# Performance work log

Measured on AMD Instinct MI355X. Metric: run time of the kernel, lower is better.

Reference implementation:

```python
import jax, jax.numpy as jnp
import numpy as np

DIM = 256
HEADS = 8
DIM_HEAD = 64
INNER = HEADS * DIM_HEAD  # 512
K = 7   # kv conv kernel == stride
P = 7   # local patch size
B = 2
N = 3584  # divisible by P and K; l = L = 512


def setup_inputs() -> dict:
    key = jax.random.key(0)
    ks = jax.random.split(key, 5)
    x = jax.random.normal(ks[0], (B, DIM, N), jnp.float32)
    # Conv1d weights (bias=False for q/kv, bias for out), kaiming-ish scale
    w_q = jax.random.normal(ks[1], (INNER, DIM), jnp.float32) * (1.0 / np.sqrt(DIM))
    w_kv = jax.random.normal(ks[2], (2 * INNER, DIM, K), jnp.float32) * (1.0 / np.sqrt(DIM * K))
    w_out = jax.random.normal(ks[3], (DIM, INNER), jnp.float32) * (1.0 / np.sqrt(INNER))
    b_out = jax.random.normal(ks[4], (DIM,), jnp.float32) * 0.01
    return {"x": x, "w_q": w_q, "w_kv": w_kv, "w_out": w_out, "b_out": b_out}


def reference(x, w_q, w_kv, w_out, b_out):
    b, c, n = x.shape
    h, d, p, kk = HEADS, DIM_HEAD, P, K
    l = n // p            # number of local query patches
    L = n // kk           # downsampled global K/V length
    scale = d ** -0.5

    # to_q: 1x1 conv (pointwise) -- same whether applied per-patch or on full seq
    q = jnp.einsum('oc,bcn->bon', w_q, x)                      # (b, inner, n)
    q = q.reshape(b, h, d, l, p).transpose(0, 3, 1, 4, 2)      # (b, l, h, p, d)

    # to_kv: Conv1d kernel=k, stride=k -> non-overlapping block contraction
    xk = x.reshape(b, c, L, kk)                                # (b, c, L, k)
    kv = jnp.einsum('ocj,bclj->bol', w_kv, xk)                 # (b, 2*inner, L)
    k_, v_ = jnp.split(kv, 2, axis=1)
    k_ = k_.reshape(b, h, d, L).transpose(0, 1, 3, 2)          # (b, h, L, d)
    v_ = v_.reshape(b, h, d, L).transpose(0, 1, 3, 2)          # (b, h, L, d)

    # Faithful to torch: q batch order is (b, l, h) while k.repeat(l,1,1)
    # gives order (l, b, h). With b | l, query (bb, ll, hh) attends to
    # K/V of batch (ll mod b), head hh. Express via reshape of l -> (l//b, b)
    # so the repeated K/V is never materialized.
    assert l % b == 0, "faithful repeat-pairing requires b | l"
    q_r = q.reshape(b, l // b, b, h, p, d)                     # e-axis = ll mod b
    dots = jnp.einsum('acehpd,ehjd->acehpj', q_r, k_) * scale  # (b, l//b, b, h, p, L)
    attn = jax.nn.softmax(dots, axis=-1)
    out = jnp.einsum('acehpj,ehjd->acehpd', attn, v_)          # (b, l//b, b, h, p, d)

    # '(b l h) p d -> b (h d) (l p)'
    out = out.reshape(b, l, h, p, d).transpose(0, 2, 4, 1, 3).reshape(b, h * d, n)

    # to_out: 1x1 conv with bias (dropout=0 -> identity)
    return jnp.einsum('oc,bcn->bon', w_out, out) + b_out[None, :, None]
```

## Files before the change

kernel.cpp:

```cpp
#include <hip/hip_runtime.h>
#include <cmath>

#define DIM 256
#define N_SEQ 3584
#define INNER 512
#define HEADS 8
#define DHEAD 64
#define LG 512
#define BATCH 2

typedef __attribute__((ext_vector_type(8))) short bf16x8;
typedef __attribute__((ext_vector_type(4))) float f32x4;

static __device__ __forceinline__ unsigned short f2b(float v) {
  unsigned u = __float_as_uint(v);
  u = u + 0x7fffu + ((u >> 16) & 1u);
  return (unsigned short)(u >> 16);
}
static __device__ __forceinline__ float b2f(unsigned short h) {
  return __uint_as_float((unsigned)h << 16);
}

#define MFMA(d, a, b) d = __builtin_amdgcn_mfma_f32_16x16x32_bf16(a, b, d, 0, 0, 0)

__global__ __launch_bounds__(256) void gemm_q(const float* __restrict__ W,
                                              const float* __restrict__ X,
                                              float* __restrict__ Q) {
  const int b  = blockIdx.z;
  const int n0 = blockIdx.x * 128;
  const int m0 = blockIdx.y * 128;
  const float* Xb = X + (size_t)b * DIM * N_SEQ;
  float* Qb = Q + (size_t)b * INNER * N_SEQ;
  __shared__ unsigned short Ah[128 * 40], Al[128 * 40];
  __shared__ unsigned short Bh[128 * 40], Bl[128 * 40];
  const int tid = threadIdx.x;
  const int lane = tid & 63, wid = tid >> 6;
  const int wr = wid >> 1, wc = wid & 1;
  const int lr = lane & 15, lk = (lane >> 4) * 8;

  f32x4 acc[4][4] = {};

  for (int k0 = 0; k0 < DIM; k0 += 32) {
    for (int i = tid; i < 4096; i += 256) {
      int kk = i & 31, mm = i >> 5;
      float v = W[(size_t)(m0 + mm) * DIM + k0 + kk];
      unsigned short h = f2b(v);
      Ah[mm * 40 + kk] = h; Al[mm * 40 + kk] = f2b(v - b2f(h));
    }
    for (int i = tid; i < 4096; i += 256) {
      int nn = i & 127, kk = i >> 7;
      float v = Xb[(size_t)(k0 + kk) * N_SEQ + n0 + nn];
      unsigned short h = f2b(v);
      Bh[nn * 40 + kk] = h; Bl[nn * 40 + kk] = f2b(v - b2f(h));
    }
    __syncthreads();
    bf16x8 ah[4], al[4], bh[4], bl[4];
    #pragma unroll
    for (int f = 0; f < 4; ++f) {
      int ar = (wr * 64 + f * 16 + lr) * 40 + lk;
      ah[f] = *(const bf16x8*)&Ah[ar]; al[f] = *(const bf16x8*)&Al[ar];
      int br = (wc * 64 + f * 16 + lr) * 40 + lk;
      bh[f] = *(const bf16x8*)&Bh[br]; bl[f] = *(const bf16x8*)&Bl[br];
    }
    #pragma unroll
    for (int fi = 0; fi < 4; ++fi)
      #pragma unroll
      for (int fj = 0; fj < 4; ++fj) {
        MFMA(acc[fi][fj], ah[fi], bh[fj]);
        MFMA(acc[fi][fj], ah[fi], bl[fj]);
        MFMA(acc[fi][fj], al[fi], bh[fj]);
      }
    __syncthreads();
  }
  const int crow = (lane >> 4) * 4, ccol = lane & 15;
  #pragma unroll
  for (int fi = 0; fi < 4; ++fi)
    #pragma unroll
    for (int fj = 0; fj < 4; ++fj) {
      int row = m0 + wr * 64 + fi * 16 + crow;
      int col = n0 + wc * 64 + fj * 16 + ccol;
      #pragma unroll
      for (int r = 0; r < 4; ++r)
        Qb[(size_t)(row + r) * N_SEQ + col] = acc[fi][fj][r];
    }
}

__global__ __launch_bounds__(256) void gemm_kv(const float* __restrict__ Wkv,
                                               const float* __restrict__ X,
                                               float* __restrict__ KVp,
                                               float* __restrict__ Pbuf) {
  const int bz = blockIdx.z;
  const int b = bz >> 2, kc = bz & 3;
  const int l0 = blockIdx.x * 64;
  const int m0 = blockIdx.y * 128;
  const int c0 = kc * 64;
  const float* Xb = X + (size_t)b * DIM * N_SEQ;
  __shared__ unsigned short Ah[128 * 72], Al[128 * 72];
  __shared__ unsigned short Bh[64 * 72],  Bl[64 * 72];
  const int tid = threadIdx.x;
  const int lane = tid & 63, wid = tid >> 6;
  const int wr = wid >> 1, wc = wid & 1;
  const int lr = lane & 15, lk = (lane >> 4) * 8;

  for (int i = tid; i < 1024; i += 256) {
    int rr = i >> 3, kk = 56 + (i & 7);
    Ah[rr * 72 + kk] = 0; Al[rr * 72 + kk] = 0;
    if (rr < 64) { Bh[rr * 72 + kk] = 0; Bl[rr * 72 + kk] = 0; }
  }

  f32x4 acc[4][2] = {};

  for (int s = 0; s < 8; ++s) {
    const int kbase = c0 * 7 + s * 56;
    const int cbase = c0 + s * 8;
    for (int i = tid; i < 7168; i += 256) {
      int kk = i % 56, mm = i / 56;
      float v = Wkv[(size_t)(m0 + mm) * 1792 + kbase + kk];
      unsigned short h = f2b(v);
      Ah[mm * 72 + kk] = h; Al[mm * 72 + kk] = f2b(v - b2f(h));
    }
    for (int i = tid; i < 3584; i += 256) {
      int ch = i / 448, t = i % 448;
      int l = t / 7, j = t - (t / 7) * 7;
      float v = Xb[(size_t)(cbase + ch) * N_SEQ + l0 * 7 + t];
      unsigned short h = f2b(v);
      int idx = l * 72 + ch * 7 + j;
      Bh[idx] = h; Bl[idx] = f2b(v - b2f(h));
    }
    __syncthreads();
    #pragma unroll
    for (int kh = 0; kh < 2; ++kh) {
      const int ko = kh * 32 + lk;
      bf16x8 ah[4], al[4], bh[2], bl[2];
      #pragma unroll
      for (int f = 0; f < 4; ++f) {
        int ar = (wr * 64 + f * 16 + lr) * 72 + ko;
        ah[f] = *(const bf16x8*)&Ah[ar]; al[f] = *(const bf16x8*)&Al[ar];
      }
      #pragma unroll
      for (int f = 0; f < 2; ++f) {
        int br = (wc * 32 + f * 16 + lr) * 72 + ko;
        bh[f] = *(const bf16x8*)&Bh[br]; bl[f] = *(const bf16x8*)&Bl[br];
      }
      #pragma unroll
      for (int fi = 0; fi < 4; ++fi)
        #pragma unroll
        for (int fj = 0; fj < 2; ++fj) {
          MFMA(acc[fi][fj], ah[fi], bh[fj]);
          MFMA(acc[fi][fj], ah[fi], bl[fj]);
          MFMA(acc[fi][fj], al[fi], bh[fj]);
        }
    }
    __syncthreads();
  }

  float* dst = (kc == 0) ? KVp : (Pbuf + (size_t)(kc - 1) * (BATCH * 2 * INNER * LG));
  dst += (size_t)b * 2 * INNER * LG;
  const int crow = (lane >> 4) * 4, ccol = lane & 15;
  #pragma unroll
  for (int fi = 0; fi < 4; ++fi)
    #pragma unroll
    for (int fj = 0; fj < 2; ++fj) {
      int row = m0 + wr * 64 + fi * 16 + crow;
      int col = l0 + wc * 32 + fj * 16 + ccol;
      #pragma unroll
      for (int r = 0; r < 4; ++r)
        dst[(size_t)(row + r) * LG + col] = acc[fi][fj][r];
    }
}

__global__ __launch_bounds__(256) void kv_reduce(float* __restrict__ KVp,
                                                 const float* __restrict__ Pbuf) {
  const size_t i = ((size_t)blockIdx.x * 256 + threadIdx.x) * 4;
  const size_t n1 = (size_t)BATCH * 2 * INNER * LG;
  float4 a  = *(const float4*)&KVp[i];
  float4 p1 = *(const float4*)&Pbuf[i];
  float4 p2 = *(const float4*)&Pbuf[n1 + i];
  float4 p3 = *(const float4*)&Pbuf[2 * n1 + i];
  a.x += p1.x + p2.x + p3.x;
  a.y += p1.y + p2.y + p3.y;
  a.z += p1.z + p2.z + p3.z;
  a.w += p1.w + p2.w + p3.w;
  *(float4*)&KVp[i] = a;
}

__global__ __launch_bounds__(256) void attn(const float* __restrict__ Q,
                                            const float* __restrict__ KV,
                                            float* __restrict__ AO) {
  const int combo = blockIdx.y;
  const int a = combo >> 4, e = (combo >> 3) & 1, h = combo & 7;
  const int r0 = blockIdx.x * 64;
  const float* Qp = Q  + ((size_t)a * INNER + h * DHEAD) * N_SEQ;
  const float* Kp = KV + ((size_t)e * 2 * INNER + h * DHEAD) * LG;
  const float* Vp = KV + ((size_t)e * 2 * INNER + INNER + h * DHEAD) * LG;
  float* Op = AO + ((size_t)a * INNER + h * DHEAD) * N_SEQ;

  __shared__ __align__(16) unsigned char smem[55296];
  unsigned short* KQh = (unsigned short*)smem;
  unsigned short* KQl = KQh + 4608;
  unsigned short* Vh_ = KQh + 2 * 4608;
  unsigned short* Vl_ = KQh + 3 * 4608;
  unsigned short* Pb  = KQh + 4 * 4608;
  float* Os = (float*)smem;

  const int tid = threadIdx.x;
  const int lane = tid & 63, w = tid >> 6;
  const int lr = lane & 15, lg = lane >> 4;
  const int lk = lg * 8;
  unsigned short* Pwh = Pb + w * 2304;
  unsigned short* Pwl = Pwh + 1152;

  for (int i = tid; i < 2048; i += 256) {
    int dp = i >> 6, r2 = i & 63, dd = dp * 2;
    int r = r0 + r2;
    int c = r / 7, p = r - c * 7;
    size_t nq = (size_t)(c * 14 + e * 7 + p);
    float q0 = Qp[(size_t)dd * N_SEQ + nq];
    float q1 = Qp[(size_t)(dd + 1) * N_SEQ + nq];
    unsigned short h0 = f2b(q0), h1 = f2b(q1);
    unsigned short u0 = f2b(q0 - b2f(h0)), u1 = f2b(q1 - b2f(h1));
    int col = dd ^ ((r2 & 7) << 3);
    *(unsigned int*)&KQh[r2 * 72 + col] = (unsigned)h0 | ((unsigned)h1 << 16);
    *(unsigned int*)&KQl[r2 * 72 + col] = (unsigned)u0 | ((unsigned)u1 << 16);
  }
  __syncthreads();
  bf16x8 qh[2], ql[2];
  {
    int base = (w * 16 + lr) * 72;
    int sw = (lr & 7) << 3;
    qh[0] = *(const bf16x8*)&KQh[base + ((0 + lk) ^ sw)];
    qh[1] = *(const bf16x8*)&KQh[base + ((32 + lk) ^ sw)];
    ql[0] = *(const bf16x8*)&KQl[base + ((0 + lk) ^ sw)];
    ql[1] = *(const bf16x8*)&KQl[base + ((32 + lk) ^ sw)];
  }

  f32x4 oacc[4] = {};
  float m_run[4] = {-INFINITY, -INFINITY, -INFINITY, -INFINITY};
  float l_run[4] = {0.f, 0.f, 0.f, 0.f};
  const float scale = 0.125f;

  for (int t = 0; t < 8; ++t) {
    const int j0 = t * 64;
    __syncthreads();
    for (int i = tid; i < 2048; i += 256) {
      int dp = i >> 6, jj = i & 63, dd = dp * 2;
      float k0v = Kp[(size_t)dd * LG + j0 + jj];
      float k1v = Kp[(size_t)(dd + 1) * LG + j0 + jj];
      unsigned short h0 = f2b(k0v), h1 = f2b(k1v);
      unsigned short u0 = f2b(k0v - b2f(h0)), u1 = f2b(k1v - b2f(h1));
      int col = dd ^ ((jj & 7) << 3);
      *(unsigned int*)&KQh[jj * 72 + col] = (unsigned)h0 | ((unsigned)h1 << 16);
      *(unsigned int*)&KQl[jj * 72 + col] = (unsigned)u0 | ((unsigned)u1 << 16);
    }
    for (int i = tid; i < 2048; i += 256) {
      int dd = i >> 5, jp = i & 31;
      float2 vv = *(const float2*)&Vp[(size_t)dd * LG + j0 + jp * 2];
      unsigned short h0 = f2b(vv.x), h1 = f2b(vv.y);
      unsigned short u0 = f2b(vv.x - b2f(h0)), u1 = f2b(vv.y - b2f(h1));
      *(unsigned int*)&Vh_[dd * 72 + jp * 2] = (unsigned)h0 | ((unsigned)h1 << 16);
      *(unsigned int*)&Vl_[dd * 72 + jp * 2] = (unsigned)u0 | ((unsigned)u1 << 16);
    }
    __syncthreads();

    f32x4 sacc[4] = {};
    #pragma unroll
    for (int ks = 0; ks < 2; ++ks) {
      #pragma unroll
      for (int f = 0; f < 4; ++f) {
        int off = (f * 16 + lr) * 72 + ((ks * 32 + lk) ^ ((lr & 7) << 3));
        bf16x8 kh = *(const bf16x8*)&KQh[off];
        bf16x8 kl = *(const bf16x8*)&KQl[off];
        MFMA(sacc[f], qh[ks], kh);
        MFMA(sacc[f], qh[ks], kl);
        MFMA(sacc[f], ql[ks], kh);
      }
    }

    float s[4][4];
    float corr[4];
    #pragma unroll
    for (int r = 0; r < 4; ++r) {
      float mx = -INFINITY;
      #pragma unroll
      for (int f = 0; f < 4; ++f) { s[f][r] = sacc[f][r] * scale; mx = fmaxf(mx, s[f][r]); }
      mx = fmaxf(mx, __shfl_xor(mx, 1));
      mx = fmaxf(mx, __shfl_xor(mx, 2));
      mx = fmaxf(mx, __shfl_xor(mx, 4));
      mx = fmaxf(mx, __shfl_xor(mx, 8));
      float mn = fmaxf(m_run[r], mx);
      corr[r] = __expf(m_run[r] - mn);
      m_run[r] = mn;
      float ls = 0.f;
      #pragma unroll
      for (int f = 0; f < 4; ++f) { s[f][r] = __expf(s[f][r] - mn); ls += s[f][r]; }
      ls += __shfl_xor(ls, 1); ls += __shfl_xor(ls, 2);
      ls += __shfl_xor(ls, 4); ls += __shfl_xor(ls, 8);
      l_run[r] = l_run[r] * corr[r] + ls;
    }

    #pragma unroll
    for (int r = 0; r < 4; ++r) {
      int prow = lg * 4 + r;
      int sw = (prow & 7) << 3;
      #pragma unroll
      for (int f = 0; f < 4; ++f) {
        int col = (16 * f + lr) ^ sw;
        unsigned short ph = f2b(s[f][r]);
        Pwh[prow * 72 + col] = ph;
        Pwl[prow * 72 + col] = f2b(s[f][r] - b2f(ph));
      }
    }
    __syncthreads();

    #pragma unroll
    for (int f = 0; f < 4; ++f)
      #pragma unroll
      for (int r = 0; r < 4; ++r)
        oacc[f][r] *= corr[r];

    #pragma unroll
    for (int ks = 0; ks < 2; ++ks) {
      int pbase = lr * 72 + ((ks * 32 + lk) ^ ((lr & 7) << 3));
      bf16x8 ph = *(const bf16x8*)&Pwh[pbase];
      bf16x8 pl = *(const bf16x8*)&Pwl[pbase];
      #pragma unroll
      for (int f = 0; f < 4; ++f) {
        int off = (f * 16 + lr) * 72 + ks * 32 + lk;
        bf16x8 vh = *(const bf16x8*)&Vh_[off];
        bf16x8 vl = *(const bf16x8*)&Vl_[off];
        MFMA(oacc[f], ph, vh);
        MFMA(oacc[f], ph, vl);
        MFMA(oacc[f], pl, vh);
      }
    }
  }

  float rl[4];
  #pragma unroll
  for (int r = 0; r < 4; ++r) rl[r] = 1.0f / l_run[r];
  #pragma unroll
  for (int f = 0; f < 4; ++f)
    #pragma unroll
    for (int r = 0; r < 4; ++r)
      Os[(w * 16 + lg * 4 + r) * 68 + 16 * f + lr] = oacc[f][r] * rl[r];
  __syncthreads();
  for (int i = tid; i < 4096; i += 256) {
    int dd = i >> 6, r2 = i & 63;
    int r = r0 + r2;
    int c = r / 7, p = r - c * 7;
    Op[(size_t)dd * N_SEQ + (c * 14 + e * 7 + p)] = Os[r2 * 68 + dd];
  }
}

__global__ __launch_bounds__(256) void gemm_out(const float* __restrict__ W,
                                                const float* __restrict__ AO,
                                                const float* __restrict__ bias,
                                                float* __restrict__ Out) {
  const int b  = blockIdx.z;
  const int n0 = blockIdx.x * 128;
  const int m0 = blockIdx.y * 64;
  const float* Ab = AO + (size_t)b * INNER * N_SEQ;
  float* Ob = Out + (size_t)b * DIM * N_SEQ;
  __shared__ unsigned short Ah[64 * 40], Al[64 * 40];
  __shared__ unsigned short Bh[128 * 40], Bl[128 * 40];
  const int tid = threadIdx.x;
  const int lane = tid & 63, wid = tid >> 6;
  const int wr = wid >> 1, wc = wid & 1;
  const int lr = lane & 15, lk = (lane >> 4) * 8;

  f32x4 acc[2][4] = {};

  for (int k0 = 0; k0 < INNER; k0 += 32) {
    for (int i = tid; i < 2048; i += 256) {
      int kk = i & 31, mm = i >> 5;
      float v = W[(size_t)(m0 + mm) * INNER + k0 + kk];
      unsigned short h = f2b(v);
      Ah[mm * 40 + kk] = h; Al[mm * 40 + kk] = f2b(v - b2f(h));
    }
    for (int i = tid; i < 4096; i += 256) {
      int nn = i & 127, kk = i >> 7;
      float v = Ab[(size_t)(k0 + kk) * N_SEQ + n0 + nn];
      unsigned short h = f2b(v);
      Bh[nn * 40 + kk] = h; Bl[nn * 40 + kk] = f2b(v - b2f(h));
    }
    __syncthreads();
    bf16x8 ah[2], al[2], bh[4], bl[4];
    #pragma unroll
    for (int f = 0; f < 2; ++f) {
      int ar = (wr * 32 + f * 16 + lr) * 40 + lk;
      ah[f] = *(const bf16x8*)&Ah[ar]; al[f] = *(const bf16x8*)&Al[ar];
    }
    #pragma unroll
    for (int f = 0; f < 4; ++f) {
      int br = (wc * 64 + f * 16 + lr) * 40 + lk;
      bh[f] = *(const bf16x8*)&Bh[br]; bl[f] = *(const bf16x8*)&Bl[br];
    }
    #pragma unroll
    for (int fi = 0; fi < 2; ++fi)
      #pragma unroll
      for (int fj = 0; fj < 4; ++fj) {
        MFMA(acc[fi][fj], ah[fi], bh[fj]);
        MFMA(acc[fi][fj], ah[fi], bl[fj]);
        MFMA(acc[fi][fj], al[fi], bh[fj]);
      }
    __syncthreads();
  }
  const int crow = (lane >> 4) * 4, ccol = lane & 15;
  #pragma unroll
  for (int fi = 0; fi < 2; ++fi)
    #pragma unroll
    for (int fj = 0; fj < 4; ++fj) {
      int row = m0 + wr * 32 + fi * 16 + crow;
      int col = n0 + wc * 64 + fj * 16 + ccol;
      #pragma unroll
      for (int r = 0; r < 4; ++r)
        Ob[(size_t)(row + r) * N_SEQ + col] = acc[fi][fj][r] + bias[row + r];
    }
}

extern "C" void kernel_launch(void* const* d_in, const int* in_sizes, int n_in,
                              void* d_out, int out_size, void* d_ws, size_t ws_size,
                              hipStream_t stream) {
  const float* x     = (const float*)d_in[0];
  const float* w_q   = (const float*)d_in[1];
  const float* w_kv  = (const float*)d_in[2];
  const float* w_out = (const float*)d_in[3];
  const float* b_out = (const float*)d_in[4];
  float* out = (float*)d_out;

  float* q_buf  = (float*)d_ws;
  float* kv_buf = q_buf + (size_t)BATCH * INNER * N_SEQ;
  float* ao_buf = kv_buf + (size_t)BATCH * 2 * INNER * LG;

  gemm_q   <<<dim3(28, 4, 2),  256, 0, stream>>>(w_q, x, q_buf);
  gemm_kv  <<<dim3(8, 8, 8),   256, 0, stream>>>(w_kv, x, kv_buf, ao_buf);
  kv_reduce<<<dim3(1024),      256, 0, stream>>>(kv_buf, ao_buf);
  attn     <<<dim3(28, 32),    256, 0, stream>>>(q_buf, kv_buf, ao_buf);
  gemm_out <<<dim3(28, 4, 2),  256, 0, stream>>>(w_out, ao_buf, b_out, out);
}
```

Before: 413.2 us.

## Fuse split-K reduction with bf16 hi/lo K/V conversion into a prep kernel

```diff
diff --git a/kernel.cpp b/kernel.cpp
--- a/kernel.cpp
+++ b/kernel.cpp
@@ -169,31 +169,73 @@
     }
 }
 
-__global__ __launch_bounds__(256) void kv_reduce(float* __restrict__ KVp,
-                                                 const float* __restrict__ Pbuf) {
-  const size_t i = ((size_t)blockIdx.x * 256 + threadIdx.x) * 4;
+__global__ __launch_bounds__(256) void kv_prep(const float* __restrict__ KVp,
+                                               const float* __restrict__ Pbuf,
+                                               unsigned short* __restrict__ Kh,
+                                               unsigned short* __restrict__ Kl,
+                                               unsigned short* __restrict__ Vh,
+                                               unsigned short* __restrict__ Vl) {
+  const int combo = blockIdx.y;
+  const int e = combo >> 3, h = combo & 7;
+  const int j0 = blockIdx.x * 64;
   const size_t n1 = (size_t)BATCH * 2 * INNER * LG;
-  float4 a  = *(const float4*)&KVp[i];
-  float4 p1 = *(const float4*)&Pbuf[i];
-  float4 p2 = *(const float4*)&Pbuf[n1 + i];
-  float4 p3 = *(const float4*)&Pbuf[2 * n1 + i];
-  a.x += p1.x + p2.x + p3.x;
-  a.y += p1.y + p2.y + p3.y;
-  a.z += p1.z + p2.z + p3.z;
-  a.w += p1.w + p2.w + p3.w;
-  *(float4*)&KVp[i] = a;
+  const size_t eoff = (size_t)e * 2 * INNER * LG;
+  const float* s0 = KVp + eoff;
+  const float* s1 = Pbuf + eoff;
+  const float* s2 = Pbuf + n1 + eoff;
+  const float* s3 = Pbuf + 2 * n1 + eoff;
+
+  __shared__ float Ls[64 * 65];
+  const int tid = threadIdx.x;
+
+  for (int i = tid; i < 4096; i += 256) {
+    int d = i >> 6, j = i & 63;
+    size_t idx = (size_t)(h * 64 + d) * LG + j0 + j;
+    Ls[d * 65 + j] = s0[idx] + s1[idx] + s2[idx] + s3[idx];
+  }
+  __syncthreads();
+  unsigned short* kh = Kh + ((size_t)combo * LG + j0) * 64;
+  unsigned short* kl = Kl + ((size_t)combo * LG + j0) * 64;
+  for (int i = tid; i < 2048; i += 256) {
+    int j = i >> 5, dp = i & 31;
+    float v0 = Ls[(2 * dp) * 65 + j];
+    float v1 = Ls[(2 * dp + 1) * 65 + j];
+    unsigned short h0 = f2b(v0), h1 = f2b(v1);
+    unsigned short u0 = f2b(v0 - b2f(h0)), u1 = f2b(v1 - b2f(h1));
+    *(unsigned int*)&kh[j * 64 + 2 * dp] = (unsigned)h0 | ((unsigned)h1 << 16);
+    *(unsigned int*)&kl[j * 64 + 2 * dp] = (unsigned)u0 | ((unsigned)u1 << 16);
+  }
+
+  unsigned short* vh = Vh + (size_t)combo * 64 * LG;
+  unsigned short* vl = Vl + (size_t)combo * 64 * LG;
+  for (int i = tid; i < 2048; i += 256) {
+    int d = i >> 5, jp = i & 31;
+    size_t idx = (size_t)(INNER + h * 64 + d) * LG + j0 + jp * 2;
+    float v0 = s0[idx] + s1[idx] + s2[idx] + s3[idx];
+    float v1 = s0[idx + 1] + s1[idx + 1] + s2[idx + 1] + s3[idx + 1];
+    unsigned short h0 = f2b(v0), h1 = f2b(v1);
+    unsigned short u0 = f2b(v0 - b2f(h0)), u1 = f2b(v1 - b2f(h1));
+    *(unsigned int*)&vh[(size_t)d * LG + j0 + jp * 2] = (unsigned)h0 | ((unsigned)h1 << 16);
+    *(unsigned int*)&vl[(size_t)d * LG + j0 + jp * 2] = (unsigned)u0 | ((unsigned)u1 << 16);
+  }
 }
 
 __global__ __launch_bounds__(256) void attn(const float* __restrict__ Q,
-                                            const float* __restrict__ KV,
+                                            const unsigned short* __restrict__ Kh,
+                                            const unsigned short* __restrict__ Kl,
+                                            const unsigned short* __restrict__ Vh,
+                                            const unsigned short* __restrict__ Vl,
                                             float* __restrict__ AO) {
   const int combo = blockIdx.y;
   const int a = combo >> 4, e = (combo >> 3) & 1, h = combo & 7;
   const int r0 = blockIdx.x * 64;
-  const float* Qp = Q  + ((size_t)a * INNER + h * DHEAD) * N_SEQ;
-  const float* Kp = KV + ((size_t)e * 2 * INNER + h * DHEAD) * LG;
-  const float* Vp = KV + ((size_t)e * 2 * INNER + INNER + h * DHEAD) * LG;
+  const float* Qp = Q + ((size_t)a * INNER + h * DHEAD) * N_SEQ;
   float* Op = AO + ((size_t)a * INNER + h * DHEAD) * N_SEQ;
+  const int cmb = e * 8 + h;
+  const unsigned short* KTh = Kh + (size_t)cmb * LG * 64;
+  const unsigned short* KTl = Kl + (size_t)cmb * LG * 64;
+  const unsigned short* VNh = Vh + (size_t)cmb * 64 * LG;
+  const unsigned short* VNl = Vl + (size_t)cmb * 64 * LG;
 
   __shared__ __align__(16) unsigned char smem[55296];
   unsigned short* KQh = (unsigned short*)smem;
@@ -242,23 +284,20 @@
   for (int t = 0; t < 8; ++t) {
     const int j0 = t * 64;
     __syncthreads();
-    for (int i = tid; i < 2048; i += 256) {
-      int dp = i >> 6, jj = i & 63, dd = dp * 2;
-      float k0v = Kp[(size_t)dd * LG + j0 + jj];
-      float k1v = Kp[(size_t)(dd + 1) * LG + j0 + jj];
-      unsigned short h0 = f2b(k0v), h1 = f2b(k1v);
-      unsigned short u0 = f2b(k0v - b2f(h0)), u1 = f2b(k1v - b2f(h1));
-      int col = dd ^ ((jj & 7) << 3);
-      *(unsigned int*)&KQh[jj * 72 + col] = (unsigned)h0 | ((unsigned)h1 << 16);
-      *(unsigned int*)&KQl[jj * 72 + col] = (unsigned)u0 | ((unsigned)u1 << 16);
-    }
-    for (int i = tid; i < 2048; i += 256) {
-      int dd = i >> 5, jp = i & 31;
-      float2 vv = *(const float2*)&Vp[(size_t)dd * LG + j0 + jp * 2];
-      unsigned short h0 = f2b(vv.x), h1 = f2b(vv.y);
-      unsigned short u0 = f2b(vv.x - b2f(h0)), u1 = f2b(vv.y - b2f(h1));
-      *(unsigned int*)&Vh_[dd * 72 + jp * 2] = (unsigned)h0 | ((unsigned)h1 << 16);
-      *(unsigned int*)&Vl_[dd * 72 + jp * 2] = (unsigned)u0 | ((unsigned)u1 << 16);
+    for (int i = tid; i < 512; i += 256) {
+      int row = i >> 3, ch = i & 7;
+      int col = (ch * 8) ^ ((row & 7) << 3);
+      *(uint4*)&KQh[row * 72 + col] =
+          *(const uint4*)&KTh[(size_t)(j0 + row) * 64 + ch * 8];
+      *(uint4*)&KQl[row * 72 + col] =
+          *(const uint4*)&KTl[(size_t)(j0 + row) * 64 + ch * 8];
+    }
+    for (int i = tid; i < 512; i += 256) {
+      int d = i >> 3, ch = i & 7;
+      *(uint4*)&Vh_[d * 72 + ch * 8] =
+          *(const uint4*)&VNh[(size_t)d * LG + j0 + ch * 8];
+      *(uint4*)&Vl_[d * 72 + ch * 8] =
+          *(const uint4*)&VNl[(size_t)d * LG + j0 + ch * 8];
     }
     __syncthreads();
 
@@ -431,10 +470,15 @@
   float* q_buf  = (float*)d_ws;
   float* kv_buf = q_buf + (size_t)BATCH * INNER * N_SEQ;
   float* ao_buf = kv_buf + (size_t)BATCH * 2 * INNER * LG;
+  unsigned short* kprep = (unsigned short*)(ao_buf + (size_t)BATCH * INNER * N_SEQ);
+  unsigned short* Kh = kprep;
+  unsigned short* Kl = Kh + (size_t)16 * LG * 64;
+  unsigned short* Vh = Kl + (size_t)16 * LG * 64;
+  unsigned short* Vl = Vh + (size_t)16 * 64 * LG;
 
   gemm_q   <<<dim3(28, 4, 2),  256, 0, stream>>>(w_q, x, q_buf);
   gemm_kv  <<<dim3(8, 8, 8),   256, 0, stream>>>(w_kv, x, kv_buf, ao_buf);
-  kv_reduce<<<dim3(1024),      256, 0, stream>>>(kv_buf, ao_buf);
-  attn     <<<dim3(28, 32),    256, 0, stream>>>(q_buf, kv_buf, ao_buf);
+  kv_prep  <<<dim3(8, 16),     256, 0, stream>>>(kv_buf, ao_buf, Kh, Kl, Vh, Vl);
+  attn     <<<dim3(28, 32),    256, 0, stream>>>(q_buf, Kh, Kl, Vh, Vl, ao_buf);
   gemm_out <<<dim3(28, 4, 2),  256, 0, stream>>>(w_out, ao_buf, b_out, out);
 }
```

Result: faster. 348.3 us (-15.7%).
